# Performance work log

Hardware: AMD Instinct MI355X
Metric: run time of the kernel (lower is better)

The kernel has to match this reference:

```python
import jax, jax.numpy as jnp
import numpy as np

H, W, C = 768, 768, 64


def _segment_ids(mask):
    """mask: [L] int binary separator mask -> [L] int32 segment ids.
    A new grid segment starts at each rising edge (0 -> 1) of the mask;
    pixel 0 always belongs to segment 0. Equivalent to GridStructureBuilder's
    run-based row/column partition, derived via a single cumsum."""
    m = mask.astype(jnp.int32)
    prev = jnp.concatenate([jnp.zeros((1,), jnp.int32), m[:-1]])
    rising = ((m == 1) & (prev == 0)).at[0].set(False)
    return jnp.cumsum(rising.astype(jnp.int32))


def setup_inputs() -> dict:
    key = jax.random.key(0)
    k1, k2, k3 = jax.random.split(key, 3)
    return {
        "input": jax.random.normal(k1, (1, H, W, C), dtype=jnp.float32),
        "h_mask": jax.random.randint(k2, (1, H), 0, 2, dtype=jnp.int32),
        "v_mask": jax.random.randint(k3, (1, W), 0, 2, dtype=jnp.int32),
    }


def reference(input, h_mask, v_mask):
    x = input[0]                      # [H, W, C]
    h, w, c = x.shape
    row_ids = _segment_ids(h_mask[0])  # [H]
    col_ids = _segment_ids(v_mask[0])  # [W]
    # flat cell id per pixel; w is a static upper bound on the column count
    idx = (row_ids[:, None] * w + col_ids[None, :]).reshape(-1)  # [H*W]
    xf = x.reshape(h * w, c)
    n_seg = h * w                      # static upper bound on cell count
    sums = jax.ops.segment_sum(xf, idx, num_segments=n_seg)           # [n_seg, C]
    counts = jax.ops.segment_sum(jnp.ones((h * w,), x.dtype), idx,
                                 num_segments=n_seg)                  # [n_seg]
    # scatter-add of (1/area)*x == per-cell mean
    means = sums / jnp.maximum(counts, 1.0)[:, None]
    # keep_size=True: gather cell means back to every pixel
    return means[idx].reshape(1, h, w, c)
```

## Files before the change

kernel.cpp:

```cpp
#include <hip/hip_runtime.h>


#define GH 768
#define GW 768
#define MAXSEG 385

typedef __attribute__((ext_vector_type(4))) float f32x4;

enum {
    OFF_ROWSTART = 0,
    OFF_ROWEND   = OFF_ROWSTART + MAXSEG,
    OFF_COLSTART = OFF_ROWEND + MAXSEG,
    OFF_COLEND   = OFF_COLSTART + MAXSEG,
    OFF_NROWS    = OFF_COLEND + MAXSEG,
    OFF_NCOLS    = OFF_NROWS + 1,
    OFF_ROWID    = OFF_NCOLS + 1,
    OFF_COLID    = OFF_ROWID + GH,
    OFF_MEANS    = 4096,
};

__global__ __launch_bounds__(768) void seg_scan(const int* __restrict__ h_mask,
                                                const int* __restrict__ v_mask,
                                                int* __restrict__ ws) {
    __shared__ int s[GH];
    const int i = threadIdx.x;
    const bool is_row = (blockIdx.x == 0);
    const int* m = is_row ? h_mask : v_mask;

    int mi = m[i];
    int rising = 0;
    if (i > 0) rising = (mi == 1 && m[i - 1] == 0) ? 1 : 0;
    s[i] = rising;
    __syncthreads();

    for (int off = 1; off < GH; off <<= 1) {
        int add = (i >= off) ? s[i - off] : 0;
        __syncthreads();
        s[i] += add;
        __syncthreads();
    }

    const int seg  = s[i];
    const int segL = (i == 0)      ? -1 : s[i - 1];
    const int segR = (i == GH - 1) ? -2 : s[i + 1];

    ws[(is_row ? OFF_ROWID : OFF_COLID) + i] = seg;

    int* start = ws + (is_row ? OFF_ROWSTART : OFF_COLSTART);
    int* end   = ws + (is_row ? OFF_ROWEND   : OFF_COLEND);
    if (seg != segL) start[seg] = i;
    if (seg != segR) end[seg]   = i + 1;
    if (i == GH - 1) ws[is_row ? OFF_NROWS : OFF_NCOLS] = seg + 1;
}

__global__ __launch_bounds__(256) void cell_mean3(const float4* __restrict__ in,
                                                  float4* __restrict__ dst,
                                                  const int* __restrict__ ws,
                                                  int anchor_mode) {
    const int nrows  = ws[OFF_NROWS];
    const int ncols  = ws[OFF_NCOLS];
    const int ncells = nrows * ncols;

    const int wave   = blockIdx.x * 4 + (threadIdx.x >> 6);
    const int nwaves = gridDim.x * 4;
    const int lane   = threadIdx.x & 63;
    const int pg     = lane >> 4;
    const int cq     = lane & 15;

    int cell = wave;
    if (cell >= ncells) return;

    int br = cell / ncols;
    int bc = cell - br * ncols;
    int y0 = ws[OFF_ROWSTART + br];
    int y1 = ws[OFF_ROWEND   + br];
    int x0 = ws[OFF_COLSTART + bc];
    int x1 = ws[OFF_COLEND   + bc];

    while (true) {
        const int ncell     = cell + nwaves;
        const bool have_next = (ncell < ncells);
        const int cc  = have_next ? ncell : 0;
        const int nbr = cc / ncols;
        const int nbc = cc - nbr * ncols;
        const int ny0 = ws[OFF_ROWSTART + nbr];
        const int ny1 = ws[OFF_ROWEND   + nbr];
        const int nx0 = ws[OFF_COLSTART + nbc];
        const int nx1 = ws[OFF_COLEND   + nbc];

        const int w    = x1 - x0;
        const int npx  = w * (y1 - y0);
        const int q    = (npx + 3) >> 2;
        const int base = pg * q;
        int len = min(base + q, npx) - base;
        const int ylim = y1 - 1;

        const unsigned ub = (unsigned)base;
        const unsigned uy = ub / (unsigned)w;
        int yy = y0 + (int)uy;
        int xx = x0 + (int)(ub - uy * (unsigned)w);

        float4 acc = make_float4(0.f, 0.f, 0.f, 0.f);

        while (len > 0) {
            const int xA = xx;           const int yAc = min(yy, ylim);
            int xB = xx + 1, yB = yy;  if (xB >= x1) { xB = x0; ++yB; }
            const int yBc = min(yB, ylim);
            int xC = xB + 1, yC = yB;  if (xC >= x1) { xC = x0; ++yC; }
            const int yCc = min(yC, ylim);
            int xD = xC + 1, yD = yC;  if (xD >= x1) { xD = x0; ++yD; }
            const int yDc = min(yD, ylim);

            const float4 vA = in[(yAc * GW + xA) * 16 + cq];
            const float4 vB = in[(yBc * GW + xB) * 16 + cq];
            const float4 vC = in[(yCc * GW + xC) * 16 + cq];
            const float4 vD = in[(yDc * GW + xD) * 16 + cq];

            const bool mB = (1 < len), mC = (2 < len), mD = (3 < len);
            acc.x += vA.x;  acc.y += vA.y;  acc.z += vA.z;  acc.w += vA.w;
            acc.x += mB ? vB.x : 0.f;  acc.y += mB ? vB.y : 0.f;
            acc.z += mB ? vB.z : 0.f;  acc.w += mB ? vB.w : 0.f;
            acc.x += mC ? vC.x : 0.f;  acc.y += mC ? vC.y : 0.f;
            acc.z += mC ? vC.z : 0.f;  acc.w += mC ? vC.w : 0.f;
            acc.x += mD ? vD.x : 0.f;  acc.y += mD ? vD.y : 0.f;
            acc.z += mD ? vD.z : 0.f;  acc.w += mD ? vD.w : 0.f;

            int xE = xD + 1, yE = yD;  if (xE >= x1) { xE = x0; ++yE; }
            xx = xE; yy = yE;
            len -= 4;
        }

        #pragma unroll
        for (int msk = 16; msk < 64; msk <<= 1) {
            acc.x += __shfl_xor(acc.x, msk, 64);
            acc.y += __shfl_xor(acc.y, msk, 64);
            acc.z += __shfl_xor(acc.z, msk, 64);
            acc.w += __shfl_xor(acc.w, msk, 64);
        }

        if (lane < 16) {
            const float inv = 1.f / (float)npx;
            float4 mean = make_float4(acc.x * inv, acc.y * inv,
                                      acc.z * inv, acc.w * inv);
            const int oidx = anchor_mode ? (y0 * GW + x0) * 16 + lane
                                         : cell * 16 + lane;
            dst[oidx] = mean;
        }

        if (!have_next) break;
        cell = ncell;
        y0 = ny0; y1 = ny1; x0 = nx0; x1 = nx1;
    }
}

__global__ __launch_bounds__(256) void bcast_ws(float4* __restrict__ out,
                                                const float4* __restrict__ means,
                                                const int* __restrict__ ws) {
    const int ncols = ws[OFF_NCOLS];
    int g = blockIdx.x * 256 + threadIdx.x;
    #pragma unroll 6
    for (int it = 0; it < 18; ++it, g += 2048 * 256) {
        const int p  = g >> 4;
        const int cq = g & 15;
        const int y  = p / GW;
        const int x  = p - y * GW;
        const int rid = ws[OFF_ROWID + y];
        const int cid = ws[OFF_COLID + x];
        const float4 v = means[(rid * ncols + cid) * 16 + cq];
        __builtin_nontemporal_store(*(const f32x4*)&v, (f32x4*)&out[g]);
    }
}

__global__ __launch_bounds__(256) void bcast_anchor(float4* out,
                                                    const int* __restrict__ ws) {
    int g = blockIdx.x * 256 + threadIdx.x;
    for (int it = 0; it < 18; ++it, g += 2048 * 256) {
        const int p  = g >> 4;
        const int cq = g & 15;
        const int y  = p / GW;
        const int x  = p - y * GW;
        const int rid = ws[OFF_ROWID + y];
        const int cid = ws[OFF_COLID + x];
        const int ya  = ws[OFF_ROWSTART + rid];
        const int xa  = ws[OFF_COLSTART + cid];
        out[g] = out[(ya * GW + xa) * 16 + cq];
    }
}

extern "C" void kernel_launch(void* const* d_in, const int* in_sizes, int n_in,
                              void* d_out, int out_size, void* d_ws, size_t ws_size,
                              hipStream_t stream) {
    const float* in  = (const float*)d_in[0];
    const int* hmask = (const int*)d_in[1];
    const int* vmask = (const int*)d_in[2];
    float* out = (float*)d_out;
    int* ws = (int*)d_ws;

    seg_scan<<<2, GH, 0, stream>>>(hmask, vmask, ws);

    const size_t need = (size_t)OFF_MEANS * 4
                      + (size_t)MAXSEG * MAXSEG * 64 * 4;
    if (ws_size >= need) {
        float4* means = (float4*)(ws + OFF_MEANS);
        cell_mean3<<<2048, 256, 0, stream>>>((const float4*)in, means, ws, 0);
        bcast_ws<<<2048, 256, 0, stream>>>((float4*)out, means, ws);
    } else {
        cell_mean3<<<2048, 256, 0, stream>>>((const float4*)in, (float4*)out, ws, 1);
        bcast_anchor<<<2048, 256, 0, stream>>>((float4*)out, ws);
    }
}
```

Measured before the change: 271.3 us.

## Split cell mean into separable row-pool and column-pool passes

Replaces the per-cell 2D reduction with two passes. The first sums each row segment down each pixel column into a rowsum buffer, with 16-column stripes per block. The second sums those rowsum entries across each column segment to get the cell means. This gives regular, coalesced streaming reads instead of per-cell scattered 2D walks with uneven work per wave. The cost is one extra kernel launch and an intermediate buffer of about 18 MB written and read back, and the path only runs when the workspace is large enough.

```diff
diff --git a/kernel.cpp b/kernel.cpp
--- a/kernel.cpp
+++ b/kernel.cpp
@@ -4,6 +4,7 @@
 #define GH 768
 #define GW 768
 #define MAXSEG 385
+#define NSTRIPE 48
 
 typedef __attribute__((ext_vector_type(4))) float f32x4;
 
@@ -18,6 +19,8 @@
     OFF_COLID    = OFF_ROWID + GH,
     OFF_MEANS    = 4096,
 };
+#define MEANS_F4  ((size_t)MAXSEG * MAXSEG * 16)
+#define ROWSUM_F4 ((size_t)MAXSEG * GW * 16)
 
 __global__ __launch_bounds__(768) void seg_scan(const int* __restrict__ h_mask,
                                                 const int* __restrict__ v_mask,
@@ -53,6 +56,116 @@
     if (i == GH - 1) ws[is_row ? OFF_NROWS : OFF_NCOLS] = seg + 1;
 }
 
+__global__ __launch_bounds__(256) void row_pool(const float4* __restrict__ in,
+                                                float4* __restrict__ rowsum,
+                                                const int* __restrict__ ws) {
+    const int nrows = ws[OFF_NROWS];
+    const int pairs = nrows * NSTRIPE;
+    const int xl = threadIdx.x >> 4;
+    const int cq = threadIdx.x & 15;
+
+    int pair = blockIdx.x;
+    if (pair >= pairs) return;
+    int rid = pair / NSTRIPE;
+    int st  = pair - rid * NSTRIPE;
+    int y0  = ws[OFF_ROWSTART + rid];
+    int y1  = ws[OFF_ROWEND   + rid];
+
+    while (true) {
+        const int npair = pair + gridDim.x;
+        const bool have_next = (npair < pairs);
+        const int pp   = have_next ? npair : 0;
+        const int nrid = pp / NSTRIPE;
+        const int nst  = pp - nrid * NSTRIPE;
+        const int ny0  = ws[OFF_ROWSTART + nrid];
+        const int ny1  = ws[OFF_ROWEND   + nrid];
+
+        const int x    = st * 16 + xl;
+        const int ylim = y1 - 1;
+        float4 acc = make_float4(0.f, 0.f, 0.f, 0.f);
+
+        for (int y = y0; y < y1; y += 4) {
+            const int yB = min(y + 1, ylim);
+            const int yC = min(y + 2, ylim);
+            const int yD = min(y + 3, ylim);
+            const float4 vA = in[((size_t)y  * GW + x) * 16 + cq];
+            const float4 vB = in[((size_t)yB * GW + x) * 16 + cq];
+            const float4 vC = in[((size_t)yC * GW + x) * 16 + cq];
+            const float4 vD = in[((size_t)yD * GW + x) * 16 + cq];
+            const bool mB = (y + 1 < y1), mC = (y + 2 < y1), mD = (y + 3 < y1);
+            acc.x += vA.x;  acc.y += vA.y;  acc.z += vA.z;  acc.w += vA.w;
+            acc.x += mB ? vB.x : 0.f;  acc.y += mB ? vB.y : 0.f;
+            acc.z += mB ? vB.z : 0.f;  acc.w += mB ? vB.w : 0.f;
+            acc.x += mC ? vC.x : 0.f;  acc.y += mC ? vC.y : 0.f;
+            acc.z += mC ? vC.z : 0.f;  acc.w += mC ? vC.w : 0.f;
+            acc.x += mD ? vD.x : 0.f;  acc.y += mD ? vD.y : 0.f;
+            acc.z += mD ? vD.z : 0.f;  acc.w += mD ? vD.w : 0.f;
+        }
+
+        rowsum[((size_t)rid * GW + x) * 16 + cq] = acc;
+
+        if (!have_next) break;
+        pair = npair; rid = nrid; st = nst; y0 = ny0; y1 = ny1;
+    }
+}
+
+__global__ __launch_bounds__(256) void col_pool(const float4* __restrict__ rowsum,
+                                                float4* __restrict__ means,
+                                                const int* __restrict__ ws) {
+    const int nrows  = ws[OFF_NROWS];
+    const int ncols  = ws[OFF_NCOLS];
+    const int ncells = nrows * ncols;
+
+    const int wave   = blockIdx.x * 4 + (threadIdx.x >> 6);
+    const int nwaves = gridDim.x * 4;
+    const int lane   = threadIdx.x & 63;
+    const int pg     = lane >> 4;
+    const int cq     = lane & 15;
+
+    int cell = wave;
+    if (cell >= ncells) return;
+    int rid = cell / ncols;
+    int cid = cell - rid * ncols;
+    int x0  = ws[OFF_COLSTART + cid];
+    int x1  = ws[OFF_COLEND   + cid];
+    int h   = ws[OFF_ROWEND + rid] - ws[OFF_ROWSTART + rid];
+
+    while (true) {
+        const int ncell = cell + nwaves;
+        const bool have_next = (ncell < ncells);
+        const int cc    = have_next ? ncell : 0;
+        const int nrid  = cc / ncols;
+        const int ncid  = cc - nrid * ncols;
+        const int nx0   = ws[OFF_COLSTART + ncid];
+        const int nx1   = ws[OFF_COLEND   + ncid];
+        const int nh    = ws[OFF_ROWEND + nrid] - ws[OFF_ROWSTART + nrid];
+
+        float4 acc = make_float4(0.f, 0.f, 0.f, 0.f);
+        const size_t rb = (size_t)rid * GW * 16 + cq;
+        for (int x = x0 + pg; x < x1; x += 4) {
+            const float4 v = rowsum[rb + (size_t)x * 16];
+            acc.x += v.x; acc.y += v.y; acc.z += v.z; acc.w += v.w;
+        }
+
+        #pragma unroll
+        for (int msk = 16; msk < 64; msk <<= 1) {
+            acc.x += __shfl_xor(acc.x, msk, 64);
+            acc.y += __shfl_xor(acc.y, msk, 64);
+            acc.z += __shfl_xor(acc.z, msk, 64);
+            acc.w += __shfl_xor(acc.w, msk, 64);
+        }
+
+        if (lane < 16) {
+            const float inv = 1.f / (float)(h * (x1 - x0));
+            means[cell * 16 + lane] = make_float4(acc.x * inv, acc.y * inv,
+                                                  acc.z * inv, acc.w * inv);
+        }
+
+        if (!have_next) break;
+        cell = ncell; rid = nrid; cid = ncid; x0 = nx0; x1 = nx1; h = nh;
+    }
+}
+
 __global__ __launch_bounds__(256) void cell_mean3(const float4* __restrict__ in,
                                                   float4* __restrict__ dst,
                                                   const int* __restrict__ ws,
@@ -69,7 +182,6 @@
 
     int cell = wave;
     if (cell >= ncells) return;
-
     int br = cell / ncols;
     int bc = cell - br * ncols;
     int y0 = ws[OFF_ROWSTART + br];
@@ -78,7 +190,7 @@
     int x1 = ws[OFF_COLEND   + bc];
 
     while (true) {
-        const int ncell     = cell + nwaves;
+        const int ncell = cell + nwaves;
         const bool have_next = (ncell < ncells);
         const int cc  = have_next ? ncell : 0;
         const int nbr = cc / ncols;
@@ -101,7 +213,6 @@
         int xx = x0 + (int)(ub - uy * (unsigned)w);
 
         float4 acc = make_float4(0.f, 0.f, 0.f, 0.f);
-
         while (len > 0) {
             const int xA = xx;           const int yAc = min(yy, ylim);
             int xB = xx + 1, yB = yy;  if (xB >= x1) { xB = x0; ++yB; }
@@ -198,9 +309,16 @@
 
     seg_scan<<<2, GH, 0, stream>>>(hmask, vmask, ws);
 
-    const size_t need = (size_t)OFF_MEANS * 4
-                      + (size_t)MAXSEG * MAXSEG * 64 * 4;
-    if (ws_size >= need) {
+    const size_t need_means = (size_t)OFF_MEANS * 4 + MEANS_F4 * 16;
+    const size_t need_full  = need_means + ROWSUM_F4 * 16;
+
+    if (ws_size >= need_full) {
+        float4* means  = (float4*)(ws + OFF_MEANS);
+        float4* rowsum = means + MEANS_F4;
+        row_pool<<<2048, 256, 0, stream>>>((const float4*)in, rowsum, ws);
+        col_pool<<<2048, 256, 0, stream>>>(rowsum, means, ws);
+        bcast_ws<<<2048, 256, 0, stream>>>((float4*)out, means, ws);
+    } else if (ws_size >= need_means) {
         float4* means = (float4*)(ws + OFF_MEANS);
         cell_mean3<<<2048, 256, 0, stream>>>((const float4*)in, means, ws, 0);
         bcast_ws<<<2048, 256, 0, stream>>>((float4*)out, means, ws);
```

Result: slower. 285.2 us (+5.1%).
